# Optimization experiments

Hardware: AMD Instinct MI355X
Metric: run time of the kernel (lower is better)

The kernel has to match this reference:

```python
import jax, jax.numpy as jnp
import numpy as np

NUM_HEADS = 16
D_MODEL = 1024


def setup_inputs() -> dict:
    key = jax.random.key(0)
    ks = jax.random.split(key, 12)
    B, S, D = 2, 2048, D_MODEL
    inp = {
        "query": jax.random.normal(ks[0], (B, S, D), dtype=jnp.float32),
        "key": jax.random.normal(ks[1], (B, S, D), dtype=jnp.float32),
        "value": jax.random.normal(ks[2], (B, S, D), dtype=jnp.float32),
        "mask": jax.random.randint(ks[3], (B, 1, S), 0, 2).astype(jnp.bool_),
    }
    # Linear layer params, stored as (in, out) so y = x @ W + b
    sd = 1.0 / np.sqrt(D)
    for i, nm in enumerate(["q", "k", "v", "o"]):
        inp[f"W{nm}"] = jax.random.uniform(ks[4 + 2 * i], (D, D), jnp.float32, -sd, sd)
        inp[f"b{nm}"] = jax.random.uniform(ks[5 + 2 * i], (D,), jnp.float32, -sd, sd)
    return inp


def _split_heads(x):
    # [B, S, D] -> [B, H, S, d_k]
    B, S, D = x.shape
    return x.reshape(B, S, NUM_HEADS, D // NUM_HEADS).transpose(0, 2, 1, 3)


def reference(query, key, value, mask, Wq, bq, Wk, bk, Wv, bv, Wo, bo):
    B, Sq, D = query.shape
    d_k = D // NUM_HEADS
    scale = 1.0 / np.sqrt(d_k)

    q = _split_heads(query @ Wq + bq)   # [B,H,Sq,dk]
    k = _split_heads(key @ Wk + bk)     # [B,H,Sk,dk]
    v = _split_heads(value @ Wv + bv)   # [B,H,Sk,dk]

    scores = jnp.einsum("bhqd,bhkd->bhqk", q, k) * scale  # [B,H,Sq,Sk]
    # mask: [B,1,Sk] bool, True = masked; broadcast over heads and queries
    scores = jnp.where(mask[:, None, :, :], -jnp.inf, scores)
    attn = jax.nn.softmax(scores, axis=-1)
    attn = jnp.nan_to_num(attn, nan=0.0)  # fully-masked rows -> 0 (matches torch)

    ctx = jnp.einsum("bhqk,bhkd->bhqd", attn, v)  # [B,H,Sq,dk]
    ctx = ctx.transpose(0, 2, 1, 3).reshape(B, Sq, D)  # combine heads
    out = ctx @ Wo + bo
    return out
```

## Files before the change

### kernel.cpp

```cpp
#include <hip/hip_runtime.h>


typedef unsigned short u16;
typedef __attribute__((ext_vector_type(8))) short bf16x8;
typedef __attribute__((ext_vector_type(4))) float f32x4;
typedef __attribute__((ext_vector_type(4))) unsigned int u32x4;
typedef __attribute__((ext_vector_type(2))) unsigned int u32x2;

static __device__ __forceinline__ u16 f2bf(float x) {
  union { float f; unsigned int i; } v; v.f = x;
  return (u16)((v.i + 0x8000u) >> 16);
}

static __device__ __forceinline__ unsigned int cvtpk(float lo, float hi) {
  unsigned int r;
  asm("v_cvt_pk_bf16_f32 %0, %1, %2" : "=v"(r) : "v"(lo), "v"(hi));
  return r;
}

static __device__ __forceinline__ void gload_lds16(const u16* g, u16* l) {
  __builtin_amdgcn_global_load_lds(
      (const __attribute__((address_space(1))) unsigned int*)g,
      (__attribute__((address_space(3))) unsigned int*)l, 16, 0, 0);
}

#define MFMA_B16(a, b, c) __builtin_amdgcn_mfma_f32_16x16x32_bf16((a), (b), (c), 0, 0, 0)

__global__ __launch_bounds__(256) void prep_w(
    const float* __restrict__ w0, const float* __restrict__ w1,
    const float* __restrict__ w2, const float* __restrict__ w3,
    u16* __restrict__ t0, u16* __restrict__ t1,
    u16* __restrict__ t2, u16* __restrict__ t3) {
  __shared__ u16 tile[64 * 68];
  const float* W; u16* T;
  switch (blockIdx.z) {
    case 0: W = w0; T = t0; break;
    case 1: W = w1; T = t1; break;
    case 2: W = w2; T = t2; break;
    default: W = w3; T = t3; break;
  }
  const int t = threadIdx.x;
  const int k0 = blockIdx.x * 64, n0 = blockIdx.y * 64;
#pragma unroll
  for (int it = 0; it < 4; ++it) {
    int idx = it * 256 + t;
    int r = idx >> 4, c4 = idx & 15;
    float4 v = *(const float4*)&W[(size_t)(k0 + r) * 1024 + n0 + c4 * 4];
    tile[r * 68 + c4 * 4 + 0] = f2bf(v.x);
    tile[r * 68 + c4 * 4 + 1] = f2bf(v.y);
    tile[r * 68 + c4 * 4 + 2] = f2bf(v.z);
    tile[r * 68 + c4 * 4 + 3] = f2bf(v.w);
  }
  __syncthreads();
#pragma unroll
  for (int it = 0; it < 2; ++it) {
    int idx = it * 256 + t;
    int n = idx >> 3, kc = idx & 7;
    bf16x8 pk;
#pragma unroll
    for (int j = 0; j < 8; ++j) pk[j] = (short)tile[(kc * 8 + j) * 68 + n];
    *(bf16x8*)&T[(size_t)(n0 + n) * 1024 + k0 + kc * 8] = pk;
  }
}

template <int MT, int AMODE, int OMODE>
__global__ __launch_bounds__(256) void gemm_bias(
    const void* a0v, const void* a1v, const void* a2v,
    const u16* __restrict__ Wt,
    const float* b0, const float* b1, const float* b2,
    void* o0, void* o1, void* o2) {
  __shared__ __align__(16) u16 As[2][MT * 32 * 32];
  __shared__ __align__(16) u16 Bs[2][128 * 32];
  const int t = threadIdx.x, wave = t >> 6, lane = t & 63;
  const int l15 = lane & 15, quad = lane >> 4;
  const int m0 = blockIdx.x * (MT * 32);
  const int n0 = blockIdx.y * 128;
  const int rg = (OMODE == 3) ? (n0 >> 10) : 0;
  const void* Av = (rg == 0) ? a0v : (rg == 1 ? a1v : a2v);
  const float* bp = (rg == 0) ? b0 : (rg == 1 ? b1 : b2);
  const int nb = (OMODE == 3) ? (n0 & 1023) : n0;
  const int wr = (wave >> 1) * (MT * 16), wc = (wave & 1) * 64;

  const f32x4 fz = {0.f, 0.f, 0.f, 0.f};
  f32x4 acc[MT][4];
#pragma unroll
  for (int mt = 0; mt < MT; ++mt)
#pragma unroll
    for (int nt = 0; nt < 4; ++nt) acc[mt][nt] = fz;

  float4 pa[MT / 2][2];

#pragma unroll
  for (int s = 0; s < 2; ++s) {
    int idx = s * 256 + t;
    gload_lds16(&Wt[(size_t)(n0 + (idx >> 2)) * 1024 + (idx & 3) * 8], &Bs[0][idx * 8]);
  }
  if (AMODE == 0) {
#pragma unroll
    for (int s = 0; s < MT / 2; ++s) {
      int idx = s * 256 + t;
      gload_lds16((const u16*)Av + (size_t)(m0 + (idx >> 2)) * 1024 + (idx & 3) * 8,
                  &As[0][idx * 8]);
    }
  } else {
#pragma unroll
    for (int s = 0; s < MT / 2; ++s) {
      int idx = s * 256 + t, row = idx >> 2, seg = idx & 3;
      const float* ap = (const float*)Av + (size_t)(m0 + row) * 1024 + seg * 8;
      pa[s][0] = *(const float4*)ap; pa[s][1] = *(const float4*)(ap + 4);
    }
#pragma unroll
    for (int s = 0; s < MT / 2; ++s) {
      int idx = s * 256 + t;
      u32x4 w;
      w[0] = cvtpk(pa[s][0].x, pa[s][0].y); w[1] = cvtpk(pa[s][0].z, pa[s][0].w);
      w[2] = cvtpk(pa[s][1].x, pa[s][1].y); w[3] = cvtpk(pa[s][1].z, pa[s][1].w);
      *(u32x4*)&As[0][idx * 8] = w;
    }
#pragma unroll
    for (int s = 0; s < MT / 2; ++s) {
      int idx = s * 256 + t, row = idx >> 2, seg = idx & 3;
      const float* ap = (const float*)Av + (size_t)(m0 + row) * 1024 + 32 + seg * 8;
      pa[s][0] = *(const float4*)ap; pa[s][1] = *(const float4*)(ap + 4);
    }
  }
  __syncthreads();

  int buf = 0;
  for (int kb = 0; kb < 1024; kb += 32) {
    const int kn = (kb + 32) & 1023;
#pragma unroll
    for (int s = 0; s < 2; ++s) {
      int idx = s * 256 + t;
      gload_lds16(&Wt[(size_t)(n0 + (idx >> 2)) * 1024 + kn + (idx & 3) * 8],
                  &Bs[buf ^ 1][idx * 8]);
    }
    if (AMODE == 0) {
#pragma unroll
      for (int s = 0; s < MT / 2; ++s) {
        int idx = s * 256 + t;
        gload_lds16((const u16*)Av + (size_t)(m0 + (idx >> 2)) * 1024 + kn + (idx & 3) * 8,
                    &As[buf ^ 1][idx * 8]);
      }
    } else {
#pragma unroll
      for (int s = 0; s < MT / 2; ++s) {
        int idx = s * 256 + t;
        u32x4 w;
        w[0] = cvtpk(pa[s][0].x, pa[s][0].y); w[1] = cvtpk(pa[s][0].z, pa[s][0].w);
        w[2] = cvtpk(pa[s][1].x, pa[s][1].y); w[3] = cvtpk(pa[s][1].z, pa[s][1].w);
        *(u32x4*)&As[buf ^ 1][idx * 8] = w;
      }
      const int kn2 = (kb + 64) & 1023;
#pragma unroll
      for (int s = 0; s < MT / 2; ++s) {
        int idx = s * 256 + t, row = idx >> 2, seg = idx & 3;
        const float* ap = (const float*)Av + (size_t)(m0 + row) * 1024 + kn2 + seg * 8;
        pa[s][0] = *(const float4*)ap; pa[s][1] = *(const float4*)(ap + 4);
      }
    }
    bf16x8 a[MT], bfr[4];
#pragma unroll
    for (int mt = 0; mt < MT; ++mt)
      a[mt] = *(const bf16x8*)&As[buf][(wr + mt * 16 + l15) * 32 + quad * 8];
#pragma unroll
    for (int nt = 0; nt < 4; ++nt)
      bfr[nt] = *(const bf16x8*)&Bs[buf][(wc + nt * 16 + l15) * 32 + quad * 8];
#pragma unroll
    for (int mt = 0; mt < MT; ++mt)
#pragma unroll
      for (int nt = 0; nt < 4; ++nt)
        acc[mt][nt] = MFMA_B16(a[mt], bfr[nt], acc[mt][nt]);
    __syncthreads();
    buf ^= 1;
  }

#pragma unroll
  for (int nt = 0; nt < 4; ++nt) {
    const int n = nb + wc + nt * 16 + l15;
    const float bv = bp[n];
#pragma unroll
    for (int mt = 0; mt < MT; ++mt)
#pragma unroll
      for (int r = 0; r < 4; ++r) {
        const int m = m0 + wr + mt * 16 + quad * 4 + r;
        const float val = acc[mt][nt][r] + bv;
        if (OMODE == 2) {
          ((float*)o0)[(size_t)m * 1024 + n] = val;
        } else if (OMODE == 0) {
          ((u16*)o0)[(size_t)m * 1024 + n] = f2bf(val);
        } else {
          if (rg == 0)      ((u16*)o0)[(size_t)m * 1024 + n] = f2bf(val);
          else if (rg == 1) ((u16*)o1)[(size_t)m * 1024 + n] = f2bf(val);
          else {
            const int h = n >> 6, d = n & 63, bb = m >> 11, ss = m & 2047;
            ((u16*)o2)[((size_t)(bb * 16 + h) * 64 + d) * 2048 + ss] = f2bf(val);
          }
        }
      }
  }
}

__global__ __launch_bounds__(512) void attn_fused(
    const u16* Q, const u16* __restrict__ K,
    const u16* __restrict__ Vt, const int* __restrict__ mask,
    u16* ctx) {
  __shared__ __align__(16) u16 Ks[128 * 72];
  __shared__ __align__(16) u16 Vs[64 * 136];
  __shared__ __align__(16) u16 Pl[8][16 * 136];
  __shared__ __align__(16) float Mf[2048];
  const int t = threadIdx.x, wave = t >> 6, lane = t & 63;
  const int l15 = lane & 15, quad = lane >> 4;
  const int bh = blockIdx.y, b = bh >> 4, h = bh & 15;
  const int q0 = blockIdx.x * 128 + wave * 16;
  const float cs = 0.125f * 1.44269504f;

#pragma unroll
  for (int i = 0; i < 4; ++i) {
    int idx = i * 512 + t;
    Mf[idx] = mask[b * 2048 + idx] ? -__builtin_inff() : 0.f;
  }

  const u16* Qp = Q + (size_t)(b * 2048 + q0) * 1024 + h * 64;
  const bf16x8 qf0 = *(const bf16x8*)(Qp + (size_t)l15 * 1024 + quad * 8);
  const bf16x8 qf1 = *(const bf16x8*)(Qp + (size_t)l15 * 1024 + 32 + quad * 8);

  const u16* Kbase = K + (size_t)(b * 2048) * 1024 + h * 64;
  const u16* Vbase = Vt + (size_t)bh * 64 * 2048;

  const int kr0 = t >> 3,        kc0 = (t & 7) * 8;
  const int kr1 = (512 + t) >> 3;
  const int vr0 = t >> 4,        vc0 = (t & 15) * 8;
  const int vr1 = (512 + t) >> 4;

  bf16x8 gk0 = *(const bf16x8*)&Kbase[(size_t)kr0 * 1024 + kc0];
  bf16x8 gk1 = *(const bf16x8*)&Kbase[(size_t)kr1 * 1024 + kc0];
  bf16x8 gv0 = *(const bf16x8*)&Vbase[(size_t)vr0 * 2048 + vc0];
  bf16x8 gv1 = *(const bf16x8*)&Vbase[(size_t)vr1 * 2048 + vc0];

  const f32x4 fz = {0.f, 0.f, 0.f, 0.f};
  f32x4 o[4];
  float lsum = 0.f;
#pragma unroll
  for (int i = 0; i < 4; ++i) o[i] = fz;

  for (int kt = 0; kt < 2048; kt += 128) {
    __syncthreads();
    *(bf16x8*)&Ks[kr0 * 72 + kc0] = gk0;
    *(bf16x8*)&Ks[kr1 * 72 + kc0] = gk1;
    *(bf16x8*)&Vs[vr0 * 136 + vc0] = gv0;
    *(bf16x8*)&Vs[vr1 * 136 + vc0] = gv1;
    __syncthreads();
    const int kn = (kt + 128) & 2047;
    gk0 = *(const bf16x8*)&Kbase[(size_t)(kn + kr0) * 1024 + kc0];
    gk1 = *(const bf16x8*)&Kbase[(size_t)(kn + kr1) * 1024 + kc0];
    gv0 = *(const bf16x8*)&Vbase[(size_t)vr0 * 2048 + kn + vc0];
    gv1 = *(const bf16x8*)&Vbase[(size_t)vr1 * 2048 + kn + vc0];

#pragma unroll
    for (int nt = 0; nt < 8; ++nt) {
      const int krow = nt * 16 + l15;
      bf16x8 k0 = *(const bf16x8*)&Ks[krow * 72 + quad * 8];
      bf16x8 k1 = *(const bf16x8*)&Ks[krow * 72 + 32 + quad * 8];
      f32x4 acc = MFMA_B16(k0, qf0, fz);
      acc = MFMA_B16(k1, qf1, acc);
      const float4 bias4 = *(const float4*)&Mf[kt + nt * 16 + quad * 4];
      float p0 = exp2f(fmaf(acc[0], cs, bias4.x));
      float p1 = exp2f(fmaf(acc[1], cs, bias4.y));
      float p2 = exp2f(fmaf(acc[2], cs, bias4.z));
      float p3 = exp2f(fmaf(acc[3], cs, bias4.w));
      lsum += (p0 + p1) + (p2 + p3);
      u32x2 pp;
      pp.x = cvtpk(p0, p1);
      pp.y = cvtpk(p2, p3);
      *(u32x2*)&Pl[wave][l15 * 136 + nt * 16 + quad * 4] = pp;
    }
#pragma unroll
    for (int kc = 0; kc < 4; ++kc) {
      const bf16x8 pf = *(const bf16x8*)&Pl[wave][l15 * 136 + kc * 32 + quad * 8];
#pragma unroll
      for (int nt = 0; nt < 4; ++nt) {
        const bf16x8 vf = *(const bf16x8*)&Vs[(nt * 16 + l15) * 136 + kc * 32 + quad * 8];
        o[nt] = MFMA_B16(pf, vf, o[nt]);
      }
    }
  }
  lsum += __shfl_xor(lsum, 16);
  lsum += __shfl_xor(lsum, 32);
  u16* cp = ctx + (size_t)(b * 2048 + q0) * 1024 + h * 64;
#pragma unroll
  for (int r = 0; r < 4; ++r) {
    const float lrow = __shfl(lsum, quad * 4 + r);
    const bool ok = lrow > 0.f;
    const float inv = ok ? 1.f / lrow : 0.f;
#pragma unroll
    for (int nt = 0; nt < 4; ++nt)
      cp[(quad * 4 + r) * 1024 + nt * 16 + l15] = f2bf(ok ? o[nt][r] * inv : 0.f);
  }
}

extern "C" void kernel_launch(void* const* d_in, const int* in_sizes, int n_in,
                              void* d_out, int out_size, void* d_ws, size_t ws_size,
                              hipStream_t stream) {
  const float* q    = (const float*)d_in[0];
  const float* k    = (const float*)d_in[1];
  const float* v    = (const float*)d_in[2];
  const int*   mask = (const int*)d_in[3];
  const float* Wq = (const float*)d_in[4];  const float* bq = (const float*)d_in[5];
  const float* Wk = (const float*)d_in[6];  const float* bk = (const float*)d_in[7];
  const float* Wv = (const float*)d_in[8];  const float* bv = (const float*)d_in[9];
  const float* Wo = (const float*)d_in[10]; const float* bo = (const float*)d_in[11];

  char* ws = (char*)d_ws;
  u16*   Kp  = (u16*)(ws + ((size_t)0 << 20));
  u16*   Vt  = (u16*)(ws + ((size_t)8 << 20));
  float* O32 = (float*)ws;

  char* od = (char*)d_out;
  u16* ctx = (u16*)od;
  u16* WqT = (u16*)(od + ((size_t)8 << 20));
  u16* WkT = (u16*)(od + ((size_t)10 << 20));
  u16* WvT = (u16*)(od + ((size_t)12 << 20));
  u16* WoT = (u16*)(od + ((size_t)14 << 20));

  dim3 blk(256);
  prep_w<<<dim3(16, 16, 4), blk, 0, stream>>>(Wq, Wk, Wv, Wo, WqT, WkT, WvT, WoT);
  gemm_bias<4, 1, 3><<<dim3(32, 24), blk, 0, stream>>>(
      q, k, v, WqT, bq, bk, bv, (void*)ctx, (void*)Kp, (void*)Vt);
  attn_fused<<<dim3(16, 32), dim3(512), 0, stream>>>(ctx, Kp, Vt, mask, ctx);
  gemm_bias<2, 0, 2><<<dim3(64, 8), blk, 0, stream>>>(
      ctx, nullptr, nullptr, WoT, bo, nullptr, nullptr, (void*)O32, nullptr, nullptr);
  hipMemcpyAsync(d_out, O32, (size_t)out_size * sizeof(float),
                 hipMemcpyDeviceToDevice, stream);
}
```

Before: 285.4 us.

## Stream fp32 activations directly to LDS via async loads, convert at fragment read

In the fp32-input GEMM path, activations were loaded into registers, converted to bf16 and stored to LDS, with a two-stage register prefetch. They are now copied as fp32 straight into LDS with global_load_lds, using an XOR swizzle on 16-byte segments to avoid bank conflicts, and converted to bf16 when each wave reads its MFMA fragments. This removes the register staging and the explicit LDS writes, and lets the A loads run asynchronously like the weight loads. In exchange it doubles the LDS footprint for A and repeats the conversion work per wave at read time.

```diff
diff --git a/kernel.cpp b/kernel.cpp
--- a/kernel.cpp
+++ b/kernel.cpp
@@ -4,7 +4,6 @@
 typedef unsigned short u16;
 typedef __attribute__((ext_vector_type(8))) short bf16x8;
 typedef __attribute__((ext_vector_type(4))) float f32x4;
-typedef __attribute__((ext_vector_type(4))) unsigned int u32x4;
 typedef __attribute__((ext_vector_type(2))) unsigned int u32x2;
 
 static __device__ __forceinline__ u16 f2bf(float x) {
@@ -18,7 +17,7 @@
   return r;
 }
 
-static __device__ __forceinline__ void gload_lds16(const u16* g, u16* l) {
+static __device__ __forceinline__ void gload_lds16(const void* g, void* l) {
   __builtin_amdgcn_global_load_lds(
       (const __attribute__((address_space(1))) unsigned int*)g,
       (__attribute__((address_space(3))) unsigned int*)l, 16, 0, 0);
@@ -69,8 +68,9 @@
     const u16* __restrict__ Wt,
     const float* b0, const float* b1, const float* b2,
     void* o0, void* o1, void* o2) {
-  __shared__ __align__(16) u16 As[2][MT * 32 * 32];
-  __shared__ __align__(16) u16 Bs[2][128 * 32];
+  __shared__ __align__(16) float Asf[(AMODE == 1) ? 2 * MT * 32 * 32 : 4];
+  __shared__ __align__(16) u16   Asb[(AMODE == 0) ? 2 * MT * 32 * 32 : 8];
+  __shared__ __align__(16) u16   Bs[2 * 128 * 32];
   const int t = threadIdx.x, wave = t >> 6, lane = t & 63;
   const int l15 = lane & 15, quad = lane >> 4;
   const int m0 = blockIdx.x * (MT * 32);
@@ -88,84 +88,62 @@
 #pragma unroll
     for (int nt = 0; nt < 4; ++nt) acc[mt][nt] = fz;
 
-  float4 pa[MT / 2][2];
-
-#pragma unroll
-  for (int s = 0; s < 2; ++s) {
-    int idx = s * 256 + t;
-    gload_lds16(&Wt[(size_t)(n0 + (idx >> 2)) * 1024 + (idx & 3) * 8], &Bs[0][idx * 8]);
-  }
-  if (AMODE == 0) {
-#pragma unroll
-    for (int s = 0; s < MT / 2; ++s) {
-      int idx = s * 256 + t;
-      gload_lds16((const u16*)Av + (size_t)(m0 + (idx >> 2)) * 1024 + (idx & 3) * 8,
-                  &As[0][idx * 8]);
-    }
-  } else {
-#pragma unroll
-    for (int s = 0; s < MT / 2; ++s) {
-      int idx = s * 256 + t, row = idx >> 2, seg = idx & 3;
-      const float* ap = (const float*)Av + (size_t)(m0 + row) * 1024 + seg * 8;
-      pa[s][0] = *(const float4*)ap; pa[s][1] = *(const float4*)(ap + 4);
-    }
-#pragma unroll
-    for (int s = 0; s < MT / 2; ++s) {
-      int idx = s * 256 + t;
-      u32x4 w;
-      w[0] = cvtpk(pa[s][0].x, pa[s][0].y); w[1] = cvtpk(pa[s][0].z, pa[s][0].w);
-      w[2] = cvtpk(pa[s][1].x, pa[s][1].y); w[3] = cvtpk(pa[s][1].z, pa[s][1].w);
-      *(u32x4*)&As[0][idx * 8] = w;
-    }
-#pragma unroll
-    for (int s = 0; s < MT / 2; ++s) {
-      int idx = s * 256 + t, row = idx >> 2, seg = idx & 3;
-      const float* ap = (const float*)Av + (size_t)(m0 + row) * 1024 + 32 + seg * 8;
-      pa[s][0] = *(const float4*)ap; pa[s][1] = *(const float4*)(ap + 4);
-    }
-  }
+#define STAGE(kk, bb)                                                           \
+  {                                                                             \
+    _Pragma("unroll")                                                           \
+    for (int s = 0; s < 2; ++s) {                                               \
+      int idx = s * 256 + t;                                                    \
+      gload_lds16(&Wt[(size_t)(n0 + (idx >> 2)) * 1024 + (kk) + (idx & 3) * 8], \
+                  &Bs[(bb) * 4096 + idx * 8]);                                  \
+    }                                                                           \
+    if (AMODE == 1) {                                                           \
+      _Pragma("unroll")                                                         \
+      for (int s = 0; s < MT; ++s) {                                            \
+        int idx = s * 256 + t, row = idx >> 3, seg = idx & 7;                   \
+        gload_lds16((const float*)Av + (size_t)(m0 + row) * 1024 + (kk) +       \
+                        ((seg ^ (row & 7)) * 4),                                \
+                    &Asf[(bb) * (MT * 32 * 32) + idx * 4]);                     \
+      }                                                                         \
+    } else {                                                                    \
+      _Pragma("unroll")                                                         \
+      for (int s = 0; s < MT / 2; ++s) {                                        \
+        int idx = s * 256 + t;                                                  \
+        gload_lds16((const u16*)Av + (size_t)(m0 + (idx >> 2)) * 1024 + (kk) +  \
+                        (idx & 3) * 8,                                          \
+                    &Asb[(bb) * (MT * 32 * 32) + idx * 8]);                     \
+      }                                                                         \
+    }                                                                           \
+  }
+
+  STAGE(0, 0);
   __syncthreads();
 
   int buf = 0;
   for (int kb = 0; kb < 1024; kb += 32) {
     const int kn = (kb + 32) & 1023;
-#pragma unroll
-    for (int s = 0; s < 2; ++s) {
-      int idx = s * 256 + t;
-      gload_lds16(&Wt[(size_t)(n0 + (idx >> 2)) * 1024 + kn + (idx & 3) * 8],
-                  &Bs[buf ^ 1][idx * 8]);
-    }
-    if (AMODE == 0) {
-#pragma unroll
-      for (int s = 0; s < MT / 2; ++s) {
-        int idx = s * 256 + t;
-        gload_lds16((const u16*)Av + (size_t)(m0 + (idx >> 2)) * 1024 + kn + (idx & 3) * 8,
-                    &As[buf ^ 1][idx * 8]);
+    STAGE(kn, buf ^ 1);
+    bf16x8 a[MT], bfr[4];
+    if (AMODE == 1) {
+      const int xr = l15 & 7;
+#pragma unroll
+      for (int mt = 0; mt < MT; ++mt) {
+        const float* base = &Asf[buf * (MT * 32 * 32) + (wr + mt * 16 + l15) * 32];
+        f32x4 a0 = *(const f32x4*)&base[((quad * 2) ^ xr) * 4];
+        f32x4 a1 = *(const f32x4*)&base[((quad * 2 + 1) ^ xr) * 4];
+        union { bf16x8 v; unsigned int w[4]; } fr;
+        fr.w[0] = cvtpk(a0[0], a0[1]); fr.w[1] = cvtpk(a0[2], a0[3]);
+        fr.w[2] = cvtpk(a1[0], a1[1]); fr.w[3] = cvtpk(a1[2], a1[3]);
+        a[mt] = fr.v;
       }
     } else {
 #pragma unroll
-      for (int s = 0; s < MT / 2; ++s) {
-        int idx = s * 256 + t;
-        u32x4 w;
-        w[0] = cvtpk(pa[s][0].x, pa[s][0].y); w[1] = cvtpk(pa[s][0].z, pa[s][0].w);
-        w[2] = cvtpk(pa[s][1].x, pa[s][1].y); w[3] = cvtpk(pa[s][1].z, pa[s][1].w);
-        *(u32x4*)&As[buf ^ 1][idx * 8] = w;
-      }
-      const int kn2 = (kb + 64) & 1023;
-#pragma unroll
-      for (int s = 0; s < MT / 2; ++s) {
-        int idx = s * 256 + t, row = idx >> 2, seg = idx & 3;
-        const float* ap = (const float*)Av + (size_t)(m0 + row) * 1024 + kn2 + seg * 8;
-        pa[s][0] = *(const float4*)ap; pa[s][1] = *(const float4*)(ap + 4);
-      }
+      for (int mt = 0; mt < MT; ++mt)
+        a[mt] = *(const bf16x8*)&Asb[buf * (MT * 32 * 32) +
+                                     (wr + mt * 16 + l15) * 32 + quad * 8];
     }
-    bf16x8 a[MT], bfr[4];
-#pragma unroll
-    for (int mt = 0; mt < MT; ++mt)
-      a[mt] = *(const bf16x8*)&As[buf][(wr + mt * 16 + l15) * 32 + quad * 8];
 #pragma unroll
     for (int nt = 0; nt < 4; ++nt)
-      bfr[nt] = *(const bf16x8*)&Bs[buf][(wc + nt * 16 + l15) * 32 + quad * 8];
+      bfr[nt] = *(const bf16x8*)&Bs[buf * 4096 + (wc + nt * 16 + l15) * 32 + quad * 8];
 #pragma unroll
     for (int mt = 0; mt < MT; ++mt)
 #pragma unroll
@@ -174,6 +152,7 @@
     __syncthreads();
     buf ^= 1;
   }
+#undef STAGE
 
 #pragma unroll
   for (int nt = 0; nt < 4; ++nt) {
```

Result: slower. 315.8 us (+10.7%).
